# Optimization experiments

Hardware: AMD Instinct MI355X
Metric: run time of the kernel (lower is better)

## Reference

```python
import jax, jax.numpy as jnp
import numpy as np
import math

D_MODEL = 256
NUM_HEADS = 8
D_HEAD = D_MODEL // NUM_HEADS


def setup_inputs() -> dict:
    key = jax.random.key(0)
    k1, k2, k3, k4, k5 = jax.random.split(key, 5)
    B, T, N = 8, 32, 256
    x = jax.random.normal(k1, (B, T, N, D_MODEL), dtype=jnp.float32)
    boxes_in_flat = jax.random.uniform(k2, (B * T * N, 4), dtype=jnp.float32)
    s = 1.0 / math.sqrt(D_MODEL)
    W_Q = jax.random.uniform(k3, (D_MODEL, D_MODEL), jnp.float32, -s, s)
    W_K = jax.random.uniform(k4, (D_MODEL, D_MODEL), jnp.float32, -s, s)
    W_V = jax.random.uniform(k5, (D_MODEL, D_MODEL), jnp.float32, -s, s)
    return {"x": x, "boxes_in_flat": boxes_in_flat, "W_Q": W_Q, "W_K": W_K, "W_V": W_V}


def reference(x, boxes_in_flat, W_Q, W_K, W_V):
    # x: [B, T, N, D]; boxes_in_flat is unused by the original forward.
    B, T, N, D = x.shape
    H, dh = NUM_HEADS, D_HEAD
    # Temporal attention pooling: softmax over T, weighted sum over T.
    t_w = jax.nn.softmax(x, axis=1)              # [B,T,N,D]
    TAtt = jnp.sum(x * t_w, axis=1)              # [B,N,D] (original tiles this over T; identical values)
    # QKV projections (nn.Linear without bias: y = x @ W^T).
    Q = (x @ W_Q.T).reshape(B, T, N, H, dh)      # [B,T,N,H,dh]
    K = (TAtt @ W_K.T).reshape(B, N, H, dh)      # [B,N,H,dh]
    V = (TAtt @ W_V.T).reshape(B, N, H, dh)      # [B,N,H,dh]
    # ReLU-scored attention with added self-loop (identity), no softmax.
    A = jnp.einsum('btnhd,bmhd->bthnm', Q, K) / jnp.sqrt(jnp.asarray(dh, x.dtype))
    A = jax.nn.relu(A) + jnp.eye(N, dtype=x.dtype)  # [B,T,H,N,N]
    out = jnp.einsum('bthnm,bmhd->btnhd', A, V)     # [B,T,N,H,dh]
    return out.reshape(B, T, N, H * dh)
```

## Files before the change

### kernel.cpp

```cpp
#include <hip/hip_runtime.h>
#include <hip/hip_bf16.h>

#define BB 8
#define TT 32
#define NN 256
#define DD 256
#define HH 8
#define DH 32

typedef __attribute__((ext_vector_type(8))) short short8v;
typedef __attribute__((ext_vector_type(4))) float f32x4;
typedef __attribute__((ext_vector_type(16))) float f32x16;
typedef __attribute__((ext_vector_type(2))) unsigned int u32x2;

static __device__ __forceinline__ unsigned short f2bfu(float f) {
    __hip_bfloat16 h = __float2bfloat16(f);
    unsigned short u;
    __builtin_memcpy(&u, &h, 2);
    return u;
}
static __device__ __forceinline__ unsigned int pkbf(float a, float b) {
    float2 f2; f2.x = a; f2.y = b;
    __hip_bfloat162 h2 = __float22bfloat162_rn(f2);
    unsigned int u;
    __builtin_memcpy(&u, &h2, 4);
    return u;
}
static __device__ __forceinline__ float bfu2f(unsigned int ubits) {
    union { unsigned int u; float f; } c;
    c.u = ubits << 16;
    return c.f;
}

__global__ __launch_bounds__(256) void wfrag_kernel(const float* __restrict__ Wq,
                                                    const float* __restrict__ Wk,
                                                    const float* __restrict__ Wv,
                                                    short* __restrict__ Wf) {
    int bid = blockIdx.x;
    int mat = bid >> 4, ctile = bid & 15;
    const float* W = (mat == 0) ? Wq : (mat == 1) ? Wk : Wv;
    short* out = Wf + (size_t)mat * (16 * 8 * 64 * 8) + (size_t)ctile * (8 * 64 * 8);
    int tid = threadIdx.x;
    int kc = tid >> 5, kg = (tid >> 3) & 3, j = tid & 7;
#pragma unroll
    for (int i = 0; i < 16; ++i) {
        float v = W[(size_t)(ctile * 16 + i) * DD + tid];
        int lane = i | (kg << 4);
        out[((size_t)kc * 64 + lane) * 8 + j] = (short)f2bfu(v);
    }
}

__global__ __launch_bounds__(1024, 1) void fused_tqkv_kernel(
        const float* __restrict__ x,
        const short* __restrict__ Wqf,
        const short* __restrict__ Wkf,
        const short* __restrict__ Wvf,
        short* __restrict__ Qb,
        short* __restrict__ Kf,
        short* __restrict__ Vf) {
    __shared__ short Xb[64][264];
    int bid = blockIdx.x;
    int b = bid >> 5;
    int n0 = (bid & 31) * 8;
    int tid = threadIdx.x;
    int w = tid >> 6, l = tid & 63;
    int lg = l >> 4, lr = l & 15;
    const f32x4 zero = {0.f, 0.f, 0.f, 0.f};

    int c = w * 16 + lr;
    int h = c >> 5, kap = c & 31;
    short8v bq[8];
#pragma unroll
    for (int kc = 0; kc < 8; ++kc)
        bq[kc] = *(const short8v*)(Wqf + (((size_t)w * 8 + kc) * 64 + l) * 8);

    int tn = tid >> 7;
    int td = (tid & 127) * 2;
    float se0 = 0.f, ws0 = 0.f, se1 = 0.f, ws1 = 0.f;

    for (int tc = 0; tc < 4; ++tc) {
        __syncthreads();
#pragma unroll
        for (int i = 0; i < 4; ++i) {
            int f = i * 1024 + tid;
            int rr = f >> 6, c4 = f & 63;
            int t = tc * 8 + (rr >> 3), n = n0 + (rr & 7);
            float4 xv = *(const float4*)(x + ((size_t)(b * TT + t) * NN + n) * DD + c4 * 4);
            short4 sv;
            sv.x = (short)f2bfu(xv.x);
            sv.y = (short)f2bfu(xv.y);
            sv.z = (short)f2bfu(xv.z);
            sv.w = (short)f2bfu(xv.w);
            *(short4*)&Xb[rr][c4 * 4] = sv;
        }
        __syncthreads();

#pragma unroll
        for (int tt = 0; tt < 8; ++tt) {
            unsigned int pr = *(const unsigned int*)&Xb[tt * 8 + tn][td];
            float v0 = bfu2f(pr & 0xFFFFu);
            float v1 = bfu2f(pr >> 16);
            float e0 = __expf(v0);
            float e1 = __expf(v1);
            se0 += e0; ws0 += v0 * e0;
            se1 += e1; ws1 += v1 * e1;
        }

#pragma unroll
        for (int rt4 = 0; rt4 < 4; ++rt4) {
            f32x4 acc = zero;
#pragma unroll
            for (int kc = 0; kc < 8; ++kc) {
                short8v a = *(const short8v*)&Xb[rt4 * 16 + lr][kc * 32 + lg * 8];
                acc = __builtin_amdgcn_mfma_f32_16x16x32_bf16(a, bq[kc], acc, 0, 0, 0);
            }
#pragma unroll
            for (int r = 0; r < 4; ++r) {
                int rowloc = rt4 * 16 + lg * 4 + r;
                int t = tc * 8 + (rowloc >> 3);
                int n = n0 + (rowloc & 7);
                size_t o = (((((size_t)(b * TT + t) * HH + h) * 8 + (n >> 5)) * 2 + (kap >> 4)) * 64
                            + (n & 31) + 32 * ((kap >> 3) & 1)) * 8 + (kap & 7);
                Qb[o] = (short)f2bfu(acc[r]);
            }
        }
    }

    __syncthreads();
    {
        float t0 = ws0 / se0;
        float t1 = ws1 / se1;
        *(unsigned int*)&Xb[tn][td] = pkbf(t0, t1);
        *(unsigned int*)&Xb[tn + 8][td] = 0u;
    }
    __syncthreads();

#pragma unroll
    for (int mat = 0; mat < 2; ++mat) {
        const short* Wfm = mat ? Wvf : Wkf;
        short8v bfr[8];
#pragma unroll
        for (int kc = 0; kc < 8; ++kc)
            bfr[kc] = *(const short8v*)(Wfm + (((size_t)w * 8 + kc) * 64 + l) * 8);
        f32x4 acc = zero;
#pragma unroll
        for (int kc = 0; kc < 8; ++kc) {
            short8v a = *(const short8v*)&Xb[lr][kc * 32 + lg * 8];
            acc = __builtin_amdgcn_mfma_f32_16x16x32_bf16(a, bfr[kc], acc, 0, 0, 0);
        }
        if (lg < 2) {
#pragma unroll
            for (int r = 0; r < 4; ++r) {
                int n = n0 + lg * 4 + r;
                if (mat == 0) {
                    float val = acc[r] * 0.17677669529663688f;
                    size_t o = ((((size_t)(b * HH + h) * 8 + (n >> 5)) * 2 + (kap >> 4)) * 64
                                + (n & 31) + 32 * ((kap >> 3) & 1)) * 8 + (kap & 7);
                    Kf[o] = (short)f2bfu(val);
                } else {
                    size_t o = ((((size_t)(b * HH + h) * 8 + (n >> 5)) * 2 + ((n >> 4) & 1)) * 64
                                + kap + 32 * ((n >> 3) & 1)) * 8 + (n & 7);
                    Vf[o] = (short)f2bfu(acc[r]);
                }
            }
        }
    }
}

__global__ __launch_bounds__(256, 4) void attn_kernel(const short* __restrict__ Qf,
                                                      const short* __restrict__ Kf,
                                                      const short* __restrict__ Vf,
                                                      float* __restrict__ out) {
    int bid = blockIdx.x;
    int h = bid & 7;
    int t = (bid >> 3) & 31;
    int b = bid >> 8;
    int tid = threadIdx.x;
    int w = tid >> 6, l = tid & 63;
    int pos = l & 31, hi = l >> 5;

    const short8v* qp = (const short8v*)Qf + ((size_t)bid * 8 + 2 * w) * 2 * 64 + l;
    short8v qf00 = qp[0];
    short8v qf01 = qp[64];
    short8v qf10 = qp[128];
    short8v qf11 = qp[192];

    const short8v* kp = (const short8v*)Kf + (size_t)(b * HH + h) * 16 * 64 + l;
    const short8v* vp = (const short8v*)Vf + (size_t)(b * HH + h) * 16 * 64 + l;

    const f32x16 z16 = {};
    f32x16 o0 = z16, o1 = z16;

#pragma unroll 2
    for (int mt = 0; mt < 8; ++mt) {
        short8v kf0 = kp[mt * 128];
        short8v kf1 = kp[mt * 128 + 64];
        short8v vf0 = vp[mt * 128];
        short8v vf1 = vp[mt * 128 + 64];
#pragma unroll
        for (int qi = 0; qi < 2; ++qi) {
            short8v qa = qi ? qf10 : qf00;
            short8v qb = qi ? qf11 : qf01;
            f32x16 p = __builtin_amdgcn_mfma_f32_32x32x16_bf16(kf0, qa, z16, 0, 0, 0);
            p = __builtin_amdgcn_mfma_f32_32x32x16_bf16(kf1, qb, p, 0, 0, 0);
#pragma unroll
            for (int r = 0; r < 16; ++r) p[r] = fmaxf(p[r], 0.f);
            if (mt == 2 * w + qi) {
#pragma unroll
                for (int r = 0; r < 16; ++r) {
                    int mloc = (r & 3) + 8 * (r >> 2) + 4 * hi;
                    if (mloc == pos) p[r] += 1.f;
                }
            }
#pragma unroll
            for (int c = 0; c < 2; ++c) {
                unsigned int A0 = pkbf(p[8 * c + 0], p[8 * c + 1]);
                unsigned int A1 = pkbf(p[8 * c + 2], p[8 * c + 3]);
                unsigned int B0 = pkbf(p[8 * c + 4], p[8 * c + 5]);
                unsigned int B1 = pkbf(p[8 * c + 6], p[8 * c + 7]);
                u32x2 s0 = __builtin_amdgcn_permlane32_swap(A0, B0, false, false);
                u32x2 s1 = __builtin_amdgcn_permlane32_swap(A1, B1, false, false);
                union { unsigned int u[4]; short8v s; } pa;
                pa.u[0] = s0[0];
                pa.u[1] = s1[0];
                pa.u[2] = s0[1];
                pa.u[3] = s1[1];
                short8v vv = c ? vf1 : vf0;
                if (qi == 0)
                    o0 = __builtin_amdgcn_mfma_f32_32x32x16_bf16(pa.s, vv, o0, 0, 0, 0);
                else
                    o1 = __builtin_amdgcn_mfma_f32_32x32x16_bf16(pa.s, vv, o1, 0, 0, 0);
            }
        }
    }

    float* ob = out + ((size_t)(b * TT + t) * NN) * DD + h * DH + pos;
#pragma unroll
    for (int r = 0; r < 16; ++r) {
        int mloc = (r & 3) + 8 * (r >> 2) + 4 * hi;
        ob[(size_t)((2 * w + 0) * 32 + mloc) * DD] = o0[r];
        ob[(size_t)((2 * w + 1) * 32 + mloc) * DD] = o1[r];
    }
}

extern "C" void kernel_launch(void* const* d_in, const int* in_sizes, int n_in,
                              void* d_out, int out_size, void* d_ws, size_t ws_size,
                              hipStream_t stream) {
    (void)in_sizes; (void)n_in; (void)out_size; (void)ws_size;
    const float* x  = (const float*)d_in[0];
    const float* Wq = (const float*)d_in[2];
    const float* Wk = (const float*)d_in[3];
    const float* Wv = (const float*)d_in[4];
    float* out = (float*)d_out;

    char* base = (char*)d_ws;
    short* Kfp = (short*)base;
    short* Vfp = (short*)(base + (size_t)1 * 1024 * 1024);
    short* Qbp = (short*)(base + (size_t)2 * 1024 * 1024);
    short* Wf  = (short*)(base + (size_t)34 * 1024 * 1024);
    short* Wqf = Wf;
    short* Wkf = Wf + (size_t)16 * 8 * 64 * 8;
    short* Wvf = Wkf + (size_t)16 * 8 * 64 * 8;

    wfrag_kernel<<<48, 256, 0, stream>>>(Wq, Wk, Wv, Wf);
    fused_tqkv_kernel<<<BB * 32, 1024, 0, stream>>>(x, Wqf, Wkf, Wvf, Qbp, Kfp, Vfp);
    attn_kernel<<<BB * TT * HH, 256, 0, stream>>>(Qbp, Kfp, Vfp, out);
}
```

Before: 158.4 us.

## Prefetch x chunks in registers, compute softmax stats in fp32, coalesce Q stores

The projection kernel now loads the next 8-timestep chunk of x into registers while the current chunk is converted and multiplied, so global latency overlaps MFMA work. The temporal softmax statistics are accumulated from the fp32 values during staging rather than re-read from bf16 shared memory, and two thread halves are reduced through shared memory. The Q tile goes through shared memory and is written as contiguous row-major 16-byte stores instead of scattered 2-byte stores into the fragment layout, and the attention kernel reads Q with strided row loads instead. This costs extra registers, extra barriers and a less contiguous Q fetch in the attention kernel.

```diff
diff --git a/kernel.cpp b/kernel.cpp
--- a/kernel.cpp
+++ b/kernel.cpp
@@ -25,11 +25,6 @@
     unsigned int u;
     __builtin_memcpy(&u, &h2, 4);
     return u;
-}
-static __device__ __forceinline__ float bfu2f(unsigned int ubits) {
-    union { unsigned int u; float f; } c;
-    c.u = ubits << 16;
-    return c.f;
 }
 
 __global__ __launch_bounds__(256) void wfrag_kernel(const float* __restrict__ Wq,
@@ -55,7 +50,7 @@
         const short* __restrict__ Wqf,
         const short* __restrict__ Wkf,
         const short* __restrict__ Wvf,
-        short* __restrict__ Qb,
+        short* __restrict__ Qg,
         short* __restrict__ Kf,
         short* __restrict__ Vf) {
     __shared__ short Xb[64][264];
@@ -68,15 +63,20 @@
     const f32x4 zero = {0.f, 0.f, 0.f, 0.f};
 
     int c = w * 16 + lr;
-    int h = c >> 5, kap = c & 31;
     short8v bq[8];
 #pragma unroll
     for (int kc = 0; kc < 8; ++kc)
         bq[kc] = *(const short8v*)(Wqf + (((size_t)w * 8 + kc) * 64 + l) * 8);
 
-    int tn = tid >> 7;
-    int td = (tid & 127) * 2;
-    float se0 = 0.f, ws0 = 0.f, se1 = 0.f, ws1 = 0.f;
+    float4 pf[4];
+#pragma unroll
+    for (int i = 0; i < 4; ++i) {
+        int f = i * 1024 + tid;
+        int rr = f >> 6, c4 = f & 63;
+        int t = (rr >> 3), n = n0 + (rr & 7);
+        pf[i] = *(const float4*)(x + ((size_t)(b * TT + t) * NN + n) * DD + c4 * 4);
+    }
+    float se[4] = {0.f, 0.f, 0.f, 0.f}, ws[4] = {0.f, 0.f, 0.f, 0.f};
 
     for (int tc = 0; tc < 4; ++tc) {
         __syncthreads();
@@ -84,57 +84,90 @@
         for (int i = 0; i < 4; ++i) {
             int f = i * 1024 + tid;
             int rr = f >> 6, c4 = f & 63;
-            int t = tc * 8 + (rr >> 3), n = n0 + (rr & 7);
-            float4 xv = *(const float4*)(x + ((size_t)(b * TT + t) * NN + n) * DD + c4 * 4);
+            float4 xv = pf[i];
             short4 sv;
             sv.x = (short)f2bfu(xv.x);
             sv.y = (short)f2bfu(xv.y);
             sv.z = (short)f2bfu(xv.z);
             sv.w = (short)f2bfu(xv.w);
             *(short4*)&Xb[rr][c4 * 4] = sv;
+            float e;
+            e = __expf(xv.x); se[0] += e; ws[0] += xv.x * e;
+            e = __expf(xv.y); se[1] += e; ws[1] += xv.y * e;
+            e = __expf(xv.z); se[2] += e; ws[2] += xv.z * e;
+            e = __expf(xv.w); se[3] += e; ws[3] += xv.w * e;
+        }
+        if (tc < 3) {
+#pragma unroll
+            for (int i = 0; i < 4; ++i) {
+                int f = i * 1024 + tid;
+                int rr = f >> 6, c4 = f & 63;
+                int t = (tc + 1) * 8 + (rr >> 3), n = n0 + (rr & 7);
+                pf[i] = *(const float4*)(x + ((size_t)(b * TT + t) * NN + n) * DD + c4 * 4);
+            }
         }
         __syncthreads();
-
-#pragma unroll
-        for (int tt = 0; tt < 8; ++tt) {
-            unsigned int pr = *(const unsigned int*)&Xb[tt * 8 + tn][td];
-            float v0 = bfu2f(pr & 0xFFFFu);
-            float v1 = bfu2f(pr >> 16);
-            float e0 = __expf(v0);
-            float e1 = __expf(v1);
-            se0 += e0; ws0 += v0 * e0;
-            se1 += e1; ws1 += v1 * e1;
-        }
-
+        f32x4 acc[4];
 #pragma unroll
         for (int rt4 = 0; rt4 < 4; ++rt4) {
-            f32x4 acc = zero;
+            acc[rt4] = zero;
 #pragma unroll
             for (int kc = 0; kc < 8; ++kc) {
                 short8v a = *(const short8v*)&Xb[rt4 * 16 + lr][kc * 32 + lg * 8];
-                acc = __builtin_amdgcn_mfma_f32_16x16x32_bf16(a, bq[kc], acc, 0, 0, 0);
-            }
-#pragma unroll
-            for (int r = 0; r < 4; ++r) {
-                int rowloc = rt4 * 16 + lg * 4 + r;
-                int t = tc * 8 + (rowloc >> 3);
-                int n = n0 + (rowloc & 7);
-                size_t o = (((((size_t)(b * TT + t) * HH + h) * 8 + (n >> 5)) * 2 + (kap >> 4)) * 64
-                            + (n & 31) + 32 * ((kap >> 3) & 1)) * 8 + (kap & 7);
-                Qb[o] = (short)f2bfu(acc[r]);
-            }
-        }
-    }
-
+                acc[rt4] = __builtin_amdgcn_mfma_f32_16x16x32_bf16(a, bq[kc], acc[rt4], 0, 0, 0);
+            }
+        }
+        __syncthreads();
+#pragma unroll
+        for (int rt4 = 0; rt4 < 4; ++rt4)
+#pragma unroll
+            for (int r = 0; r < 4; ++r)
+                Xb[rt4 * 16 + lg * 4 + r][c] = (short)f2bfu(acc[rt4][r]);
+        __syncthreads();
+#pragma unroll
+        for (int i = 0; i < 2; ++i) {
+            int f = i * 1024 + tid;
+            int row = f >> 5, cq = f & 31;
+            int t = tc * 8 + (row >> 3), n = n0 + (row & 7);
+            short8v qv = *(const short8v*)&Xb[row][cq * 8];
+            *(short8v*)(Qg + ((size_t)(b * TT + t) * NN + n) * 256 + cq * 8) = qv;
+        }
+    }
+
+    __syncthreads();
+    float* scratch = (float*)&Xb[0][0];
+    if (tid >= 512) {
+        int part = tid & 511;
+#pragma unroll
+        for (int j = 0; j < 4; ++j) {
+            scratch[part * 8 + j] = se[j];
+            scratch[part * 8 + 4 + j] = ws[j];
+        }
+    }
+    __syncthreads();
+    float tv[4] = {0.f, 0.f, 0.f, 0.f};
+    if (tid < 512) {
+#pragma unroll
+        for (int j = 0; j < 4; ++j) {
+            float s = se[j] + scratch[tid * 8 + j];
+            float v = ws[j] + scratch[tid * 8 + 4 + j];
+            tv[j] = v / s;
+        }
+    }
     __syncthreads();
     {
-        float t0 = ws0 / se0;
-        float t1 = ws1 / se1;
-        *(unsigned int*)&Xb[tn][td] = pkbf(t0, t1);
-        *(unsigned int*)&Xb[tn + 8][td] = 0u;
+        int n = (tid >> 6) & 7, c4 = tid & 63;
+        if (tid < 512) {
+            *(unsigned int*)&Xb[n][c4 * 4] = pkbf(tv[0], tv[1]);
+            *(unsigned int*)&Xb[n][c4 * 4 + 2] = pkbf(tv[2], tv[3]);
+        } else {
+            *(unsigned int*)&Xb[8 + n][c4 * 4] = 0u;
+            *(unsigned int*)&Xb[8 + n][c4 * 4 + 2] = 0u;
+        }
     }
     __syncthreads();
 
+    int h = c >> 5, kap = c & 31;
 #pragma unroll
     for (int mat = 0; mat < 2; ++mat) {
         const short* Wfm = mat ? Wvf : Wkf;
@@ -167,7 +200,7 @@
     }
 }
 
-__global__ __launch_bounds__(256, 4) void attn_kernel(const short* __restrict__ Qf,
+__global__ __launch_bounds__(256, 4) void attn_kernel(const short* __restrict__ Qg,
                                                       const short* __restrict__ Kf,
                                                       const short* __restrict__ Vf,
                                                       float* __restrict__ out) {
@@ -179,11 +212,11 @@
     int w = tid >> 6, l = tid & 63;
     int pos = l & 31, hi = l >> 5;
 
-    const short8v* qp = (const short8v*)Qf + ((size_t)bid * 8 + 2 * w) * 2 * 64 + l;
-    short8v qf00 = qp[0];
-    short8v qf01 = qp[64];
-    short8v qf10 = qp[128];
-    short8v qf11 = qp[192];
+    const short* qlane = Qg + ((size_t)(b * TT + t) * NN) * 256 + h * 32 + pos * 256 + hi * 8;
+    short8v qf00 = *(const short8v*)(qlane + (2 * w + 0) * 8192);
+    short8v qf01 = *(const short8v*)(qlane + (2 * w + 0) * 8192 + 16);
+    short8v qf10 = *(const short8v*)(qlane + (2 * w + 1) * 8192);
+    short8v qf11 = *(const short8v*)(qlane + (2 * w + 1) * 8192 + 16);
 
     const short8v* kp = (const short8v*)Kf + (size_t)(b * HH + h) * 16 * 64 + l;
     const short8v* vp = (const short8v*)Vf + (size_t)(b * HH + h) * 16 * 64 + l;
@@ -213,11 +246,11 @@
                 }
             }
 #pragma unroll
-            for (int c = 0; c < 2; ++c) {
-                unsigned int A0 = pkbf(p[8 * c + 0], p[8 * c + 1]);
-                unsigned int A1 = pkbf(p[8 * c + 2], p[8 * c + 3]);
-                unsigned int B0 = pkbf(p[8 * c + 4], p[8 * c + 5]);
-                unsigned int B1 = pkbf(p[8 * c + 6], p[8 * c + 7]);
+            for (int cc = 0; cc < 2; ++cc) {
+                unsigned int A0 = pkbf(p[8 * cc + 0], p[8 * cc + 1]);
+                unsigned int A1 = pkbf(p[8 * cc + 2], p[8 * cc + 3]);
+                unsigned int B0 = pkbf(p[8 * cc + 4], p[8 * cc + 5]);
+                unsigned int B1 = pkbf(p[8 * cc + 6], p[8 * cc + 7]);
                 u32x2 s0 = __builtin_amdgcn_permlane32_swap(A0, B0, false, false);
                 u32x2 s1 = __builtin_amdgcn_permlane32_swap(A1, B1, false, false);
                 union { unsigned int u[4]; short8v s; } pa;
@@ -225,7 +258,7 @@
                 pa.u[1] = s1[0];
                 pa.u[2] = s0[1];
                 pa.u[3] = s1[1];
-                short8v vv = c ? vf1 : vf0;
+                short8v vv = cc ? vf1 : vf0;
                 if (qi == 0)
                     o0 = __builtin_amdgcn_mfma_f32_32x32x16_bf16(pa.s, vv, o0, 0, 0, 0);
                 else
@@ -256,13 +289,13 @@
     char* base = (char*)d_ws;
     short* Kfp = (short*)base;
     short* Vfp = (short*)(base + (size_t)1 * 1024 * 1024);
-    short* Qbp = (short*)(base + (size_t)2 * 1024 * 1024);
-    short* Wf  = (short*)(base + (size_t)34 * 1024 * 1024);
+    short* Qgp = (short*)(base + (size_t)2 * 1024 * 1024);
+    short* Wf  = (short*)(base + (size_t)36 * 1024 * 1024);
     short* Wqf = Wf;
     short* Wkf = Wf + (size_t)16 * 8 * 64 * 8;
     short* Wvf = Wkf + (size_t)16 * 8 * 64 * 8;
 
     wfrag_kernel<<<48, 256, 0, stream>>>(Wq, Wk, Wv, Wf);
-    fused_tqkv_kernel<<<BB * 32, 1024, 0, stream>>>(x, Wqf, Wkf, Wvf, Qbp, Kfp, Vfp);
-    attn_kernel<<<BB * TT * HH, 256, 0, stream>>>(Qbp, Kfp, Vfp, out);
-}
+    fused_tqkv_kernel<<<BB * 32, 1024, 0, stream>>>(x, Wqf, Wkf, Wvf, Qgp, Kfp, Vfp);
+    attn_kernel<<<BB * TT * HH, 256, 0, stream>>>(Qgp, Kfp, Vfp, out);
+}
```

Result: slower. 163.5 us (+3.2%).
